# Optimization experiments

Hardware: AMD Instinct MI355X
Metric: run time of the kernel (lower is better)

Reference implementation:

```python
import jax, jax.numpy as jnp
import numpy as np

NEG = -9e15
SLOPE = 0.1  # LeakyReLU negative_slope in the torch module

B, N, NFEAT = 4, 2048, 256
NHID, NHEADS, NOUT = 64, 8, 128


def setup_inputs() -> dict:
    key = jax.random.key(0)
    ks = jax.random.split(key, 8)
    x = jax.random.normal(ks[0], (B, N, NFEAT), dtype=jnp.float32)
    adj = jax.random.randint(ks[1], (B, N, N), 0, 2, dtype=jnp.int32)
    s = 0.1
    Wh = jax.random.normal(ks[2], (NHEADS, NFEAT, NHID), dtype=jnp.float32) * s
    ah = jax.random.normal(ks[3], (NHEADS, 2 * NHID), dtype=jnp.float32) * s
    bh = jax.random.normal(ks[4], (NHEADS, NHID), dtype=jnp.float32) * s
    Wo = jax.random.normal(ks[5], (NHID * NHEADS, NOUT), dtype=jnp.float32) * s
    ao = jax.random.normal(ks[6], (2 * NOUT,), dtype=jnp.float32) * s
    bo = jax.random.normal(ks[7], (NOUT,), dtype=jnp.float32) * s
    return {"x": x, "adj": adj, "Wh": Wh, "ah": ah, "bh": bh,
            "Wo": Wo, "ao": ao, "bo": bo}


def _leaky(v):
    return jnp.where(v >= 0, v, SLOPE * v)


def _gat_layer(x, adj, W, a, b):
    # x: [B,N,Fin], W: [Fin,F], a: [2F], b: [F]
    h = jnp.einsum('bnf,fo->bno', x, W)          # [B,N,F]
    F = W.shape[1]
    a1, a2 = a[:F], a[F:]
    s1 = h @ a1                                   # [B,N] (query / row term)
    s2 = h @ a2                                   # [B,N] (key / col term)
    e = _leaky(s1[:, :, None] + s2[:, None, :])   # [B,N,N], avoids a_input blowup
    e = jnp.where(adj > 0, e, NEG)
    att = jax.nn.softmax(e, axis=2)               # [B,N,N]
    h_prime = jnp.einsum('bnm,bmf->bnf', att, h) + b
    return jax.nn.elu(h_prime)


def reference(x, adj, Wh, ah, bh, Wo, ao, bo):
    # per-head layers, vmapped over the head axis of the stacked params
    heads = jax.vmap(lambda W, a, b: _gat_layer(x, adj, W, a, b))(Wh, ah, bh)
    # [H,B,N,F] -> concat heads along feature dim: [B,N,H*F]
    hcat = jnp.transpose(heads, (1, 2, 0, 3)).reshape(x.shape[0], x.shape[1], -1)
    out = _gat_layer(hcat, adj, Wo, ao, bo)
    return jax.nn.relu(out)
```

## Files before the change

kernel.cpp:

```cpp
#include <hip/hip_runtime.h>

constexpr int B_ = 4;
constexpr int N_ = 2048;
constexpr int NFEAT_ = 256;
constexpr int NHEADS_ = 8;
constexpr float SLOPE_ = 0.1f;
constexpr float L2E = 1.4426950408889634f;

typedef __attribute__((ext_vector_type(8))) __fp16 f16x8;
typedef __attribute__((ext_vector_type(4))) __fp16 f16x4;
typedef __attribute__((ext_vector_type(2))) __fp16 f16x2;
typedef __attribute__((ext_vector_type(4))) float f32x4;

__device__ __forceinline__ f16x8 pack8(const float* v) {
  union { f16x2 h2[4]; f16x8 h8; } u;
  u.h2[0] = __builtin_amdgcn_cvt_pkrtz(v[0], v[1]);
  u.h2[1] = __builtin_amdgcn_cvt_pkrtz(v[2], v[3]);
  u.h2[2] = __builtin_amdgcn_cvt_pkrtz(v[4], v[5]);
  u.h2[3] = __builtin_amdgcn_cvt_pkrtz(v[6], v[7]);
  return u.h8;
}
__device__ __forceinline__ f16x4 pack4(float a, float b, float c, float d) {
  union { f16x2 h2[2]; f16x4 h4; } u;
  u.h2[0] = __builtin_amdgcn_cvt_pkrtz(a, b);
  u.h2[1] = __builtin_amdgcn_cvt_pkrtz(c, d);
  return u.h4;
}

__global__ __launch_bounds__(256) void k_prep(
    const int* __restrict__ adj, unsigned short* __restrict__ mask2,
    const float* __restrict__ Wh, __fp16* __restrict__ WhB,
    const float* __restrict__ Wo, __fp16* __restrict__ WoB)
{
  const int bid = blockIdx.x;
  const int l = threadIdx.x & 63;
  if (bid < 4096) {
    const size_t gw = ((size_t)bid * 256 + threadIdx.x) >> 6;
    const int jt = (int)(gw & 31);
    const int ig16 = (int)((gw >> 5) & 127);
    const int b = (int)(gw >> 12);
    const int q = l >> 4, c15 = l & 15;
    const int* base = adj + ((size_t)b * N_ + ig16 * 16) * N_ + jt * 64 + l;
    unsigned int msk = 0;
    #pragma unroll
    for (int r = 0; r < 16; ++r) {
      int a = base[(size_t)r * N_];
      unsigned long long bal = __ballot(a > 0);
      unsigned int v = (unsigned int)((bal >> (q * 8)) & 0xffull)
                     | ((unsigned int)((bal >> (q * 8 + 32)) & 0xffull) << 8);
      if (r == c15) msk = v;
    }
    mask2[gw * 64 + l] = (unsigned short)msk;
  } else if (bid < 4160) {
    int s = (int)(((bid - 4096) * 256 + threadIdx.x) >> 6);
    int h = s >> 5, ks = (s >> 2) & 7, ft = s & 3;
    const float* src = Wh + ((size_t)h * 256 + ks * 32 + (l >> 4) * 8) * 64 + ft * 16 + (l & 15);
    float v[8];
    #pragma unroll
    for (int j = 0; j < 8; ++j) v[j] = src[(size_t)j * 64];
    *(f16x8*)(WhB + (size_t)s * 512 + l * 8) = pack8(v);
  } else {
    int s = (int)(((bid - 4160) * 256 + threadIdx.x) >> 6);
    int ks = s >> 3, ft = s & 7;
    const float* src = Wo + ((size_t)ks * 32 + (l >> 4) * 8) * 128 + ft * 16 + (l & 15);
    float v[8];
    #pragma unroll
    for (int j = 0; j < 8; ++j) v[j] = src[(size_t)j * 128];
    *(f16x8*)(WoB + (size_t)s * 512 + l * 8) = pack8(v);
  }
}

__global__ __launch_bounds__(256, 4) void k_gemm1(
    const float* __restrict__ x, const __fp16* __restrict__ WhB,
    const float* __restrict__ ah,
    __fp16* __restrict__ hB1, float* __restrict__ s1h, float* __restrict__ s2h)
{
  constexpr int XP = 264;
  __shared__ __fp16 xs[16 * XP];
  __shared__ __fp16 hT[512 * 16];

  const int t = threadIdx.x;
  const int bid = blockIdx.x;
  const int b = bid >> 7;
  const int n0 = (bid & 127) * 16;

  {
    int r = t >> 4, k0 = (t & 15) * 16;
    const float* src = x + ((size_t)(b * N_) + n0 + r) * NFEAT_ + k0;
    float v0[8], v1[8];
    *(float4*)&v0[0] = *(const float4*)(src);
    *(float4*)&v0[4] = *(const float4*)(src + 4);
    *(float4*)&v1[0] = *(const float4*)(src + 8);
    *(float4*)&v1[4] = *(const float4*)(src + 12);
    *(f16x8*)&xs[r * XP + k0] = pack8(v0);
    *(f16x8*)&xs[r * XP + k0 + 8] = pack8(v1);
  }
  __syncthreads();

  const int w = t >> 6, l = t & 63;
  const int quad = l >> 4, c15 = l & 15;

  f32x4 acc[8];
  #pragma unroll
  for (int i = 0; i < 8; ++i) acc[i] = (f32x4){0.f, 0.f, 0.f, 0.f};

  for (int ks = 0; ks < 8; ++ks) {
    f16x8 af = *(const f16x8*)&xs[c15 * XP + ks * 32 + quad * 8];
    #pragma unroll
    for (int tt = 0; tt < 8; ++tt) {
      int hl = tt >> 2, ft = tt & 3;
      f16x8 bf = *(const f16x8*)(WhB +
          ((((size_t)(2 * w + hl) * 8 + ks) * 4 + ft) * 512) + l * 8);
      acc[tt] = __builtin_amdgcn_mfma_f32_16x16x32_f16(af, bf, acc[tt], 0, 0, 0);
    }
  }

  #pragma unroll
  for (int hl = 0; hl < 2; ++hl) {
    int head = 2 * w + hl;
    float a1v[4], a2v[4];
    #pragma unroll
    for (int ft = 0; ft < 4; ++ft) {
      a1v[ft] = ah[head * 128 + ft * 16 + c15] * L2E;
      a2v[ft] = ah[head * 128 + 64 + ft * 16 + c15] * L2E;
    }
    #pragma unroll
    for (int r = 0; r < 4; ++r) {
      float v1 = 0.f, v2 = 0.f;
      #pragma unroll
      for (int ft = 0; ft < 4; ++ft) {
        v1 = fmaf(acc[hl * 4 + ft][r], a1v[ft], v1);
        v2 = fmaf(acc[hl * 4 + ft][r], a2v[ft], v2);
      }
      #pragma unroll
      for (int off = 1; off < 16; off <<= 1) {
        v1 += __shfl_xor(v1, off, 64);
        v2 += __shfl_xor(v2, off, 64);
      }
      if (c15 == 0) {
        s1h[(size_t)(b * NHEADS_ + head) * N_ + n0 + quad * 4 + r] = v1;
        s2h[(size_t)(b * NHEADS_ + head) * N_ + n0 + quad * 4 + r] = v2;
      }
    }
  }

  #pragma unroll
  for (int tt = 0; tt < 8; ++tt) {
    int f = (2 * w + (tt >> 2)) * 64 + (tt & 3) * 16 + c15;
    *(f16x4*)&hT[f * 16 + quad * 4] =
        pack4(acc[tt][0], acc[tt][1], acc[tt][2], acc[tt][3]);
  }
  __syncthreads();

  const int base_oct = (n0 >> 3) & 3;
  #pragma unroll
  for (int q = 0; q < 4; ++q) {
    int s = t + q * 256;
    int c15v = s & 15, oct = (s >> 4) & 1, ft = (s >> 5) & 3, head = s >> 7;
    f16x8 v = *(const f16x8*)&hT[(head * 64 + ft * 16 + c15v) * 16 + oct * 8];
    int lane0 = (base_oct + oct) * 16 + c15v;
    *(f16x8*)(hB1 +
        ((((size_t)(b * NHEADS_ + head) * 64 + (n0 >> 5)) * 4 + ft) * 512) + lane0 * 8) = v;
  }
}

__global__ __launch_bounds__(256, 4) void k_gemm2(
    const __fp16* __restrict__ g1, const __fp16* __restrict__ WoB,
    const float* __restrict__ ao,
    __fp16* __restrict__ hB2, float* __restrict__ s1o, float* __restrict__ s2o)
{
  constexpr int GP = 520;
  __shared__ __fp16 gs[16 * GP];
  __shared__ __fp16 hT[128 * 16];
  __shared__ float sd1[4][16], sd2[4][16];

  const int t = threadIdx.x;
  const int bid = blockIdx.x;
  const int b = bid >> 7;
  const int n0 = (bid & 127) * 16;

  {
    int r = t >> 4, k0 = (t & 15) * 32;
    const __fp16* src = g1 + ((size_t)(b * N_) + n0 + r) * 512 + k0;
    #pragma unroll
    for (int i = 0; i < 4; ++i)
      *(f16x8*)&gs[r * GP + k0 + i * 8] = *(const f16x8*)(src + i * 8);
  }
  __syncthreads();

  const int w = t >> 6, l = t & 63;
  const int quad = l >> 4, c15 = l & 15;

  f32x4 acc[2];
  acc[0] = (f32x4){0.f, 0.f, 0.f, 0.f};
  acc[1] = (f32x4){0.f, 0.f, 0.f, 0.f};

  for (int ks = 0; ks < 16; ++ks) {
    f16x8 af = *(const f16x8*)&gs[c15 * GP + ks * 32 + quad * 8];
    #pragma unroll
    for (int tt = 0; tt < 2; ++tt) {
      int ft = 2 * w + tt;
      f16x8 bf = *(const f16x8*)(WoB + (((size_t)ks * 8 + ft) * 512) + l * 8);
      acc[tt] = __builtin_amdgcn_mfma_f32_16x16x32_f16(af, bf, acc[tt], 0, 0, 0);
    }
  }

  {
    float a1v[2], a2v[2];
    #pragma unroll
    for (int tt = 0; tt < 2; ++tt) {
      int f = (2 * w + tt) * 16 + c15;
      a1v[tt] = ao[f] * L2E;
      a2v[tt] = ao[128 + f] * L2E;
    }
    #pragma unroll
    for (int r = 0; r < 4; ++r) {
      float v1 = acc[0][r] * a1v[0] + acc[1][r] * a1v[1];
      float v2 = acc[0][r] * a2v[0] + acc[1][r] * a2v[1];
      #pragma unroll
      for (int off = 1; off < 16; off <<= 1) {
        v1 += __shfl_xor(v1, off, 64);
        v2 += __shfl_xor(v2, off, 64);
      }
      if (c15 == 0) { sd1[w][quad * 4 + r] = v1; sd2[w][quad * 4 + r] = v2; }
    }
  }

  #pragma unroll
  for (int tt = 0; tt < 2; ++tt) {
    int f = (2 * w + tt) * 16 + c15;
    *(f16x4*)&hT[f * 16 + quad * 4] =
        pack4(acc[tt][0], acc[tt][1], acc[tt][2], acc[tt][3]);
  }
  __syncthreads();

  if (t < 16)
    s1o[(size_t)b * N_ + n0 + t] = sd1[0][t] + sd1[1][t] + sd1[2][t] + sd1[3][t];
  else if (t < 32) {
    int rr = t - 16;
    s2o[(size_t)b * N_ + n0 + rr] = sd2[0][rr] + sd2[1][rr] + sd2[2][rr] + sd2[3][rr];
  }

  {
    int c15v = t & 15, oct = (t >> 4) & 1, ft = t >> 5;
    f16x8 v = *(const f16x8*)&hT[(ft * 16 + c15v) * 16 + oct * 8];
    int base_oct = (n0 >> 3) & 3;
    int lane0 = (base_oct + oct) * 16 + c15v;
    *(f16x8*)(hB2 +
        (((size_t)(b * 64 + (n0 >> 5)) * 8 + ft) * 512) + lane0 * 8) = v;
  }
}

__global__ __launch_bounds__(512, 4) void k_att1(
    const __fp16* __restrict__ hB, const float* __restrict__ s1,
    const float* __restrict__ s2, const unsigned short* __restrict__ mask2,
    const float* __restrict__ bias, __fp16* __restrict__ g1)
{
  constexpr int NRG = 4, NJQ = 2, JLEN = 1024, TJ = 64, NIT = JLEN / TJ;
  constexpr int TILE = TJ * 64;

  __shared__ __fp16 vbuf[NJQ][2][TILE];
  __shared__ float s2s[N_];
  __shared__ float red[8];

  const int tid = threadIdx.x;
  const int w = tid >> 6, l = tid & 63;
  const int quad = l >> 4, c15 = l & 15;
  const int rowg = w % NRG, jq = w / NRG;
  const int tc = rowg * 64 + l;

  int idx = blockIdx.x;
  const int ig = idx & 31; idx >>= 5;
  const int head = idx & 7;
  const int b = idx >> 3;
  const int i0w = ig * 64 + rowg * 16;

  const float* s1p = s1 + (size_t)(b * 8 + head) * N_;
  const float* s2p = s2 + (size_t)(b * 8 + head) * N_;
  const char* hBp = (const char*)(hB + (size_t)(b * 8 + head) * (N_ / 32) * 2048);
  const unsigned short* mp = mask2 + ((size_t)(b * 128 + (i0w >> 4)) * 32) * 64 + l;

  const int jbase = jq * JLEN;

  auto stage = [&](int j0, int slot) {
    const char* srcb = hBp + (size_t)(j0 >> 5) * 4096;
    #pragma unroll
    for (int c = 0; c < 2; ++c) {
      int off = (tc + c * 256) * 16;
      __builtin_amdgcn_global_load_lds(
          (const __attribute__((address_space(1))) unsigned int*)(srcb + off),
          (__attribute__((address_space(3))) unsigned int*)
              ((char*)&vbuf[jq][slot][0] + (off - l * 16)), 16, 0, 0);
    }
  };

  stage(jbase, 0);
  unsigned int mk = mp[(size_t)(jbase >> 6) * 64];

  float4 sv = *(const float4*)(s2p + tid * 4);
  *(float4*)&s2s[tid * 4] = sv;
  float lm = fmaxf(fmaxf(sv.x, sv.y), fmaxf(sv.z, sv.w));
  #pragma unroll
  for (int off = 1; off < 64; off <<= 1) lm = fmaxf(lm, __shfl_xor(lm, off, 64));
  if (l == 0) red[w] = lm;
  const float s1v = s1p[i0w + c15];
  __syncthreads();
  float s2m = red[0];
  #pragma unroll
  for (int q = 1; q < 8; ++q) s2m = fmaxf(s2m, red[q]);

  const float zm = s1v + s2m;
  const float m = fmaxf(zm, SLOPE_ * zm);
  const float p = s1v - m;
  const float cq = (SLOPE_ - 1.f) * m;

  f16x8 ones;
  #pragma unroll
  for (int i = 0; i < 8; ++i) ones[i] = (__fp16)1.0f;

  f32x4 acc[4], acc5;
  #pragma unroll
  for (int t = 0; t < 4; ++t) acc[t] = (f32x4){0.f, 0.f, 0.f, 0.f};
  acc5 = (f32x4){0.f, 0.f, 0.f, 0.f};

  for (int it = 0; it < NIT; ++it) {
    const int cur = it & 1;
    const int j0 = jbase + it * TJ;
    unsigned int nk = 0;
    if (it + 1 < NIT) {
      stage(j0 + TJ, cur ^ 1);
      nk = mp[(size_t)((j0 + TJ) >> 6) * 64];
    }

    #pragma unroll
    for (int h = 0; h < 2; ++h) {
      const int jk = j0 + h * 32;
      float s2r[8];
      *(float4*)&s2r[0] = *(const float4*)&s2s[jk + quad * 8];
      *(float4*)&s2r[4] = *(const float4*)&s2s[jk + quad * 8 + 4];
      const unsigned int mbyte = (mk >> (8 * h)) & 0xffu;
      float wgt[8];
      #pragma unroll
      for (int k = 0; k < 8; ++k) {
        float t0 = p + s2r[k];
        float t1 = fmaf(SLOPE_, t0, cq);
        float tm = fmaxf(t0, t1);
        float e = __builtin_amdgcn_exp2f(tm);
        int sel = (int)(mbyte << (31 - k)) >> 31;
        union { float f; int i; } u; u.f = e; u.i &= sel;
        wgt[k] = u.f;
      }
      f16x8 a = pack8(wgt);
      acc5 = __builtin_amdgcn_mfma_f32_16x16x32_f16(a, ones, acc5, 0, 0, 0);
      const __fp16* vb = &vbuf[jq][cur][h * 2048];
      #pragma unroll
      for (int t = 0; t < 4; ++t) {
        f16x8 bf = *(const f16x8*)(vb + t * 512 + l * 8);
        acc[t] = __builtin_amdgcn_mfma_f32_16x16x32_f16(a, bf, acc[t], 0, 0, 0);
      }
    }
    mk = nk;
    __syncthreads();
  }

  auto pacc = (float(*)[16][64])(&vbuf[0][0][0]);
  auto pls  = (float(*)[16])(&s2s[0]);
  if (jq == 1) {
    #pragma unroll
    for (int t = 0; t < 4; ++t)
      #pragma unroll
      for (int r = 0; r < 4; ++r)
        pacc[rowg][quad * 4 + r][t * 16 + c15] = acc[t][r];
    if (c15 == 0) {
      #pragma unroll
      for (int r = 0; r < 4; ++r) pls[rowg][quad * 4 + r] = acc5[r];
    }
  }
  __syncthreads();
  if (jq == 0) {
    float Lrow[4];
    #pragma unroll
    for (int r = 0; r < 4; ++r)
      Lrow[r] = acc5[r] + pls[rowg][quad * 4 + r];
    #pragma unroll
    for (int t = 0; t < 4; ++t)
      #pragma unroll
      for (int r = 0; r < 4; ++r)
        acc[t][r] += pacc[rowg][quad * 4 + r][t * 16 + c15];
    float lr[4];
    #pragma unroll
    for (int r = 0; r < 4; ++r) lr[r] = 1.f / Lrow[r];
    #pragma unroll
    for (int t = 0; t < 4; ++t) {
      const float bv = bias[head * 64 + t * 16 + c15];
      #pragma unroll
      for (int r = 0; r < 4; ++r) {
        const int i = i0w + quad * 4 + r;
        float v = acc[t][r] * lr[r] + bv;
        v = (v > 0.f) ? v : expm1f(v);
        g1[(size_t)(b * N_ + i) * 512 + head * 64 + t * 16 + c15] = (__fp16)v;
      }
    }
  }
}

__global__ __launch_bounds__(512, 4) void k_att2(
    const __fp16* __restrict__ hB, const float* __restrict__ s1,
    const float* __restrict__ s2, const unsigned short* __restrict__ mask2,
    const float* __restrict__ bias, float* __restrict__ out)
{
  constexpr int NRG = 2, NJQ = 4, JLEN = 512, TJ = 32, NIT = JLEN / TJ;
  constexpr int TILE = TJ * 64;

  __shared__ __fp16 vbuf[NJQ][2][TILE];
  __shared__ float s2s[N_];
  __shared__ float red[8];

  const int tid = threadIdx.x;
  const int w = tid >> 6, l = tid & 63;
  const int quad = l >> 4, c15 = l & 15;
  const int rowg = w % NRG, jq = w / NRG;
  const int tc = rowg * 64 + l;

  int idx = blockIdx.x;
  const int ig = idx & 63; idx >>= 6;
  const int fs = idx & 1;
  const int b = idx >> 1;
  const int i0w = ig * 32 + rowg * 16;

  const float* s1p = s1 + (size_t)b * N_;
  const float* s2p = s2 + (size_t)b * N_;
  const char* hBp = (const char*)(hB + (size_t)b * 64 * 4096 + fs * 2048);
  const unsigned short* mp = mask2 + ((size_t)(b * 128 + (i0w >> 4)) * 32) * 64 + l;

  const int jbase = jq * JLEN;

  auto stage = [&](int j0, int slot) {
    const char* srcb = hBp + (size_t)(j0 >> 5) * 8192;
    #pragma unroll
    for (int c = 0; c < 2; ++c) {
      int off = (tc + c * 128) * 16;
      __builtin_amdgcn_global_load_lds(
          (const __attribute__((address_space(1))) unsigned int*)(srcb + off),
          (__attribute__((address_space(3))) unsigned int*)
              ((char*)&vbuf[jq][slot][0] + (off - l * 16)), 16, 0, 0);
    }
  };

  stage(jbase, 0);
  unsigned int mk = mp[(size_t)(jbase >> 6) * 64];

  float4 sv = *(const float4*)(s2p + tid * 4);
  *(float4*)&s2s[tid * 4] = sv;
  float lm = fmaxf(fmaxf(sv.x, sv.y), fmaxf(sv.z, sv.w));
  #pragma unroll
  for (int off = 1; off < 64; off <<= 1) lm = fmaxf(lm, __shfl_xor(lm, off, 64));
  if (l == 0) red[w] = lm;
  const float s1v = s1p[i0w + c15];
  __syncthreads();
  float s2m = red[0];
  #pragma unroll
  for (int q = 1; q < 8; ++q) s2m = fmaxf(s2m, red[q]);

  const float zm = s1v + s2m;
  const float m = fmaxf(zm, SLOPE_ * zm);
  const float p = s1v - m;
  const float cq = (SLOPE_ - 1.f) * m;

  f16x8 ones;
  #pragma unroll
  for (int i = 0; i < 8; ++i) ones[i] = (__fp16)1.0f;

  f32x4 acc[4], acc5;
  #pragma unroll
  for (int t = 0; t < 4; ++t) acc[t] = (f32x4){0.f, 0.f, 0.f, 0.f};
  acc5 = (f32x4){0.f, 0.f, 0.f, 0.f};

  for (int it = 0; it < NIT; ++it) {
    const int cur = it & 1;
    const int j0 = jbase + it * TJ;
    unsigned int nk = 0;
    if (it + 1 < NIT) {
      stage(j0 + TJ, cur ^ 1);
      nk = mp[(size_t)((j0 + TJ) >> 6) * 64];
    }

    float s2r[8];
    *(float4*)&s2r[0] = *(const float4*)&s2s[j0 + quad * 8];
    *(float4*)&s2r[4] = *(const float4*)&s2s[j0 + quad * 8 + 4];
    const unsigned int mbyte = (mk >> (8 * ((j0 >> 5) & 1))) & 0xffu;
    float wgt[8];
    #pragma unroll
    for (int k = 0; k < 8; ++k) {
      float t0 = p + s2r[k];
      float t1 = fmaf(SLOPE_, t0, cq);
      float tm = fmaxf(t0, t1);
      float e = __builtin_amdgcn_exp2f(tm);
      int sel = (int)(mbyte << (31 - k)) >> 31;
      union { float f; int i; } u; u.f = e; u.i &= sel;
      wgt[k] = u.f;
    }
    f16x8 a = pack8(wgt);
    acc5 = __builtin_amdgcn_mfma_f32_16x16x32_f16(a, ones, acc5, 0, 0, 0);
    const __fp16* vb = &vbuf[jq][cur][0];
    #pragma unroll
    for (int t = 0; t < 4; ++t) {
      f16x8 bf = *(const f16x8*)(vb + t * 512 + l * 8);
      acc[t] = __builtin_amdgcn_mfma_f32_16x16x32_f16(a, bf, acc[t], 0, 0, 0);
    }
    mk = nk;
    __syncthreads();
  }

  auto pacc = (float(*)[NRG][16][64])(&vbuf[0][0][0]);
  auto pls  = (float(*)[NRG][16])(&s2s[0]);
  if (jq > 0) {
    #pragma unroll
    for (int t = 0; t < 4; ++t)
      #pragma unroll
      for (int r = 0; r < 4; ++r)
        pacc[jq - 1][rowg][quad * 4 + r][t * 16 + c15] = acc[t][r];
    if (c15 == 0) {
      #pragma unroll
      for (int r = 0; r < 4; ++r) pls[jq - 1][rowg][quad * 4 + r] = acc5[r];
    }
  }
  __syncthreads();
  if (jq == 0) {
    float Lrow[4];
    #pragma unroll
    for (int r = 0; r < 4; ++r) Lrow[r] = acc5[r];
    #pragma unroll
    for (int q = 0; q < NJQ - 1; ++q) {
      #pragma unroll
      for (int t = 0; t < 4; ++t)
        #pragma unroll
        for (int r = 0; r < 4; ++r)
          acc[t][r] += pacc[q][rowg][quad * 4 + r][t * 16 + c15];
      #pragma unroll
      for (int r = 0; r < 4; ++r) Lrow[r] += pls[q][rowg][quad * 4 + r];
    }
    float lr[4];
    #pragma unroll
    for (int r = 0; r < 4; ++r) lr[r] = 1.f / Lrow[r];
    #pragma unroll
    for (int t = 0; t < 4; ++t) {
      const float bv = bias[fs * 64 + t * 16 + c15];
      #pragma unroll
      for (int r = 0; r < 4; ++r) {
        const int i = i0w + quad * 4 + r;
        float v = acc[t][r] * lr[r] + bv;
        out[(size_t)(b * N_ + i) * 128 + fs * 64 + t * 16 + c15] = fmaxf(v, 0.f);
      }
    }
  }
}

extern "C" void kernel_launch(void* const* d_in, const int* in_sizes, int n_in,
                              void* d_out, int out_size, void* d_ws, size_t ws_size,
                              hipStream_t stream) {
  const float* x   = (const float*)d_in[0];
  const int*   adj = (const int*)d_in[1];
  const float* Wh  = (const float*)d_in[2];
  const float* ah  = (const float*)d_in[3];
  const float* bh  = (const float*)d_in[4];
  const float* Wo  = (const float*)d_in[5];
  const float* ao  = (const float*)d_in[6];
  const float* bo  = (const float*)d_in[7];
  float* out = (float*)d_out;

  float* ws   = (float*)d_ws;
  float* s1h  = ws;
  float* s2h  = s1h  + (size_t)B_ * NHEADS_ * N_;
  float* s1o  = s2h  + (size_t)B_ * NHEADS_ * N_;
  float* s2o  = s1o  + (size_t)B_ * N_;
  __fp16* g1  = (__fp16*)(s2o + (size_t)B_ * N_);
  __fp16* hB1 = g1  + (size_t)B_ * N_ * 512;
  __fp16* hB2 = hB1 + (size_t)B_ * NHEADS_ * N_ * 64;
  __fp16* WhB = hB2 + (size_t)B_ * N_ * 128;
  __fp16* WoB = WhB + (size_t)8 * 256 * 64;
  unsigned short* mask2 = (unsigned short*)(WoB + (size_t)512 * 128);

  k_prep<<<4192, 256, 0, stream>>>(adj, mask2, Wh, WhB, Wo, WoB);
  k_gemm1<<<B_ * (N_ / 16), 256, 0, stream>>>(x, WhB, ah, hB1, s1h, s2h);
  k_att1<<<B_ * NHEADS_ * (N_ / 64), 512, 0, stream>>>(
      hB1, s1h, s2h, mask2, bh, g1);
  k_gemm2<<<B_ * (N_ / 16), 256, 0, stream>>>(g1, WoB, ao, hB2, s1o, s2o);
  k_att2<<<B_ * 2 * (N_ / 32), 512, 0, stream>>>(
      hB2, s1o, s2o, mask2, bo, out);
}
```

Measured before the change: 198.1 us.

## Load value tiles directly from global into registers, dropping LDS double buffering

Both attention kernels stop staging the pre-swizzled h tiles into shared memory through async global-to-LDS copies with double buffering and per-iteration barriers. Each wave now loads its MFMA B-operand fragments straight from global memory (relying on L2/L1 reuse across waves and blocks), and the loop no longer needs __syncthreads. The partial-result reduction buffers become dedicated shared arrays instead of aliasing the old staging buffer. This removes barrier stalls and LDS traffic, but every wave now issues redundant global loads and latency hiding depends on the compiler and occupancy.

```diff
diff --git a/kernel.cpp b/kernel.cpp
--- a/kernel.cpp
+++ b/kernel.cpp
@@ -256,18 +256,17 @@
     const float* __restrict__ s2, const unsigned short* __restrict__ mask2,
     const float* __restrict__ bias, __fp16* __restrict__ g1)
 {
-  constexpr int NRG = 4, NJQ = 2, JLEN = 1024, TJ = 64, NIT = JLEN / TJ;
-  constexpr int TILE = TJ * 64;
-
-  __shared__ __fp16 vbuf[NJQ][2][TILE];
+  constexpr int NRG = 4, NJQ = 2, JLEN = 1024;
+
   __shared__ float s2s[N_];
   __shared__ float red[8];
+  __shared__ float pacc[NRG][16][64];
+  __shared__ float pls[NRG][16];
 
   const int tid = threadIdx.x;
   const int w = tid >> 6, l = tid & 63;
   const int quad = l >> 4, c15 = l & 15;
   const int rowg = w % NRG, jq = w / NRG;
-  const int tc = rowg * 64 + l;
 
   int idx = blockIdx.x;
   const int ig = idx & 31; idx >>= 5;
@@ -277,25 +276,10 @@
 
   const float* s1p = s1 + (size_t)(b * 8 + head) * N_;
   const float* s2p = s2 + (size_t)(b * 8 + head) * N_;
-  const char* hBp = (const char*)(hB + (size_t)(b * 8 + head) * (N_ / 32) * 2048);
+  const __fp16* hBp = hB + (size_t)(b * 8 + head) * (N_ / 32) * 2048 + l * 8;
   const unsigned short* mp = mask2 + ((size_t)(b * 128 + (i0w >> 4)) * 32) * 64 + l;
 
   const int jbase = jq * JLEN;
-
-  auto stage = [&](int j0, int slot) {
-    const char* srcb = hBp + (size_t)(j0 >> 5) * 4096;
-    #pragma unroll
-    for (int c = 0; c < 2; ++c) {
-      int off = (tc + c * 256) * 16;
-      __builtin_amdgcn_global_load_lds(
-          (const __attribute__((address_space(1))) unsigned int*)(srcb + off),
-          (__attribute__((address_space(3))) unsigned int*)
-              ((char*)&vbuf[jq][slot][0] + (off - l * 16)), 16, 0, 0);
-    }
-  };
-
-  stage(jbase, 0);
-  unsigned int mk = mp[(size_t)(jbase >> 6) * 64];
 
   float4 sv = *(const float4*)(s2p + tid * 4);
   *(float4*)&s2s[tid * 4] = sv;
@@ -323,18 +307,17 @@
   for (int t = 0; t < 4; ++t) acc[t] = (f32x4){0.f, 0.f, 0.f, 0.f};
   acc5 = (f32x4){0.f, 0.f, 0.f, 0.f};
 
-  for (int it = 0; it < NIT; ++it) {
-    const int cur = it & 1;
-    const int j0 = jbase + it * TJ;
-    unsigned int nk = 0;
-    if (it + 1 < NIT) {
-      stage(j0 + TJ, cur ^ 1);
-      nk = mp[(size_t)((j0 + TJ) >> 6) * 64];
-    }
-
+  for (int it = 0; it < JLEN / 64; ++it) {
+    const int j0 = jbase + it * 64;
+    const unsigned int mk = mp[(size_t)(j0 >> 6) * 64];
     #pragma unroll
     for (int h = 0; h < 2; ++h) {
       const int jk = j0 + h * 32;
+      const __fp16* vb = hBp + (size_t)(jk >> 5) * 2048;
+      f16x8 bf0 = *(const f16x8*)(vb);
+      f16x8 bf1 = *(const f16x8*)(vb + 512);
+      f16x8 bf2 = *(const f16x8*)(vb + 1024);
+      f16x8 bf3 = *(const f16x8*)(vb + 1536);
       float s2r[8];
       *(float4*)&s2r[0] = *(const float4*)&s2s[jk + quad * 8];
       *(float4*)&s2r[4] = *(const float4*)&s2s[jk + quad * 8 + 4];
@@ -352,19 +335,13 @@
       }
       f16x8 a = pack8(wgt);
       acc5 = __builtin_amdgcn_mfma_f32_16x16x32_f16(a, ones, acc5, 0, 0, 0);
-      const __fp16* vb = &vbuf[jq][cur][h * 2048];
-      #pragma unroll
-      for (int t = 0; t < 4; ++t) {
-        f16x8 bf = *(const f16x8*)(vb + t * 512 + l * 8);
-        acc[t] = __builtin_amdgcn_mfma_f32_16x16x32_f16(a, bf, acc[t], 0, 0, 0);
-      }
-    }
-    mk = nk;
-    __syncthreads();
-  }
-
-  auto pacc = (float(*)[16][64])(&vbuf[0][0][0]);
-  auto pls  = (float(*)[16])(&s2s[0]);
+      acc[0] = __builtin_amdgcn_mfma_f32_16x16x32_f16(a, bf0, acc[0], 0, 0, 0);
+      acc[1] = __builtin_amdgcn_mfma_f32_16x16x32_f16(a, bf1, acc[1], 0, 0, 0);
+      acc[2] = __builtin_amdgcn_mfma_f32_16x16x32_f16(a, bf2, acc[2], 0, 0, 0);
+      acc[3] = __builtin_amdgcn_mfma_f32_16x16x32_f16(a, bf3, acc[3], 0, 0, 0);
+    }
+  }
+
   if (jq == 1) {
     #pragma unroll
     for (int t = 0; t < 4; ++t)
@@ -409,18 +386,17 @@
     const float* __restrict__ s2, const unsigned short* __restrict__ mask2,
     const float* __restrict__ bias, float* __restrict__ out)
 {
-  constexpr int NRG = 2, NJQ = 4, JLEN = 512, TJ = 32, NIT = JLEN / TJ;
-  constexpr int TILE = TJ * 64;
-
-  __shared__ __fp16 vbuf[NJQ][2][TILE];
+  constexpr int NRG = 2, NJQ = 4, JLEN = 512;
+
   __shared__ float s2s[N_];
   __shared__ float red[8];
+  __shared__ float pacc[NJQ - 1][NRG][16][64];
+  __shared__ float pls[NJQ - 1][NRG][16];
 
   const int tid = threadIdx.x;
   const int w = tid >> 6, l = tid & 63;
   const int quad = l >> 4, c15 = l & 15;
   const int rowg = w % NRG, jq = w / NRG;
-  const int tc = rowg * 64 + l;
 
   int idx = blockIdx.x;
   const int ig = idx & 63; idx >>= 6;
@@ -430,25 +406,10 @@
 
   const float* s1p = s1 + (size_t)b * N_;
   const float* s2p = s2 + (size_t)b * N_;
-  const char* hBp = (const char*)(hB + (size_t)b * 64 * 4096 + fs * 2048);
+  const __fp16* hBp = hB + (size_t)b * 64 * 4096 + fs * 2048 + l * 8;
   const unsigned short* mp = mask2 + ((size_t)(b * 128 + (i0w >> 4)) * 32) * 64 + l;
 
   const int jbase = jq * JLEN;
-
-  auto stage = [&](int j0, int slot) {
-    const char* srcb = hBp + (size_t)(j0 >> 5) * 8192;
-    #pragma unroll
-    for (int c = 0; c < 2; ++c) {
-      int off = (tc + c * 128) * 16;
-      __builtin_amdgcn_global_load_lds(
-          (const __attribute__((address_space(1))) unsigned int*)(srcb + off),
-          (__attribute__((address_space(3))) unsigned int*)
-              ((char*)&vbuf[jq][slot][0] + (off - l * 16)), 16, 0, 0);
-    }
-  };
-
-  stage(jbase, 0);
-  unsigned int mk = mp[(size_t)(jbase >> 6) * 64];
 
   float4 sv = *(const float4*)(s2p + tid * 4);
   *(float4*)&s2s[tid * 4] = sv;
@@ -476,44 +437,41 @@
   for (int t = 0; t < 4; ++t) acc[t] = (f32x4){0.f, 0.f, 0.f, 0.f};
   acc5 = (f32x4){0.f, 0.f, 0.f, 0.f};
 
-  for (int it = 0; it < NIT; ++it) {
-    const int cur = it & 1;
-    const int j0 = jbase + it * TJ;
-    unsigned int nk = 0;
-    if (it + 1 < NIT) {
-      stage(j0 + TJ, cur ^ 1);
-      nk = mp[(size_t)((j0 + TJ) >> 6) * 64];
-    }
-
-    float s2r[8];
-    *(float4*)&s2r[0] = *(const float4*)&s2s[j0 + quad * 8];
-    *(float4*)&s2r[4] = *(const float4*)&s2s[j0 + quad * 8 + 4];
-    const unsigned int mbyte = (mk >> (8 * ((j0 >> 5) & 1))) & 0xffu;
-    float wgt[8];
-    #pragma unroll
-    for (int k = 0; k < 8; ++k) {
-      float t0 = p + s2r[k];
-      float t1 = fmaf(SLOPE_, t0, cq);
-      float tm = fmaxf(t0, t1);
-      float e = __builtin_amdgcn_exp2f(tm);
-      int sel = (int)(mbyte << (31 - k)) >> 31;
-      union { float f; int i; } u; u.f = e; u.i &= sel;
-      wgt[k] = u.f;
-    }
-    f16x8 a = pack8(wgt);
-    acc5 = __builtin_amdgcn_mfma_f32_16x16x32_f16(a, ones, acc5, 0, 0, 0);
-    const __fp16* vb = &vbuf[jq][cur][0];
-    #pragma unroll
-    for (int t = 0; t < 4; ++t) {
-      f16x8 bf = *(const f16x8*)(vb + t * 512 + l * 8);
-      acc[t] = __builtin_amdgcn_mfma_f32_16x16x32_f16(a, bf, acc[t], 0, 0, 0);
-    }
-    mk = nk;
-    __syncthreads();
-  }
-
-  auto pacc = (float(*)[NRG][16][64])(&vbuf[0][0][0]);
-  auto pls  = (float(*)[NRG][16])(&s2s[0]);
+  for (int it = 0; it < JLEN / 64; ++it) {
+    const int j0 = jbase + it * 64;
+    const unsigned int mk = mp[(size_t)(j0 >> 6) * 64];
+    #pragma unroll
+    for (int h = 0; h < 2; ++h) {
+      const int jk = j0 + h * 32;
+      const __fp16* vb = hBp + (size_t)(jk >> 5) * 4096;
+      f16x8 bf0 = *(const f16x8*)(vb);
+      f16x8 bf1 = *(const f16x8*)(vb + 512);
+      f16x8 bf2 = *(const f16x8*)(vb + 1024);
+      f16x8 bf3 = *(const f16x8*)(vb + 1536);
+      float s2r[8];
+      *(float4*)&s2r[0] = *(const float4*)&s2s[jk + quad * 8];
+      *(float4*)&s2r[4] = *(const float4*)&s2s[jk + quad * 8 + 4];
+      const unsigned int mbyte = (mk >> (8 * h)) & 0xffu;
+      float wgt[8];
+      #pragma unroll
+      for (int k = 0; k < 8; ++k) {
+        float t0 = p + s2r[k];
+        float t1 = fmaf(SLOPE_, t0, cq);
+        float tm = fmaxf(t0, t1);
+        float e = __builtin_amdgcn_exp2f(tm);
+        int sel = (int)(mbyte << (31 - k)) >> 31;
+        union { float f; int i; } u; u.f = e; u.i &= sel;
+        wgt[k] = u.f;
+      }
+      f16x8 a = pack8(wgt);
+      acc5 = __builtin_amdgcn_mfma_f32_16x16x32_f16(a, ones, acc5, 0, 0, 0);
+      acc[0] = __builtin_amdgcn_mfma_f32_16x16x32_f16(a, bf0, acc[0], 0, 0, 0);
+      acc[1] = __builtin_amdgcn_mfma_f32_16x16x32_f16(a, bf1, acc[1], 0, 0, 0);
+      acc[2] = __builtin_amdgcn_mfma_f32_16x16x32_f16(a, bf2, acc[2], 0, 0, 0);
+      acc[3] = __builtin_amdgcn_mfma_f32_16x16x32_f16(a, bf3, acc[3], 0, 0, 0);
+    }
+  }
+
   if (jq > 0) {
     #pragma unroll
     for (int t = 0; t < 4; ++t)
```

After: 209.9 us. +5.9%, slower.

## Compute attention weights in packed fp16 and stage V via registers

Applied to the files above, without the earlier changes.

Replaces the per-element fp32 LeakyReLU/exp2/mask chain with packed half-precision v_pk_fma/v_pk_max and v_exp_f16 through inline asm, using a small shared-memory LUT to expand mask bits into 16-bit lane masks. Also swaps the direct global-to-LDS async loads for register prefetch of the next V tile, written to LDS after the MFMAs. The goal is fewer VALU instructions per weight in the softmax-numerator path. In exchange it loses fp16 range and precision in the exponent argument and adds register pressure plus explicit LDS store traffic.

```diff
diff --git a/kernel.cpp b/kernel.cpp
--- a/kernel.cpp
+++ b/kernel.cpp
@@ -25,6 +25,23 @@
   u.h2[0] = __builtin_amdgcn_cvt_pkrtz(a, b);
   u.h2[1] = __builtin_amdgcn_cvt_pkrtz(c, d);
   return u.h4;
+}
+
+__device__ __forceinline__ unsigned int wpair(float za, float zb,
+                                              f16x2 sl2, f16x2 cq2,
+                                              unsigned int pm) {
+  f16x2 t0 = __builtin_amdgcn_cvt_pkrtz(za, zb);
+  f16x2 t1, tm;
+  asm("v_pk_fma_f16 %0, %1, %2, %3" : "=v"(t1) : "v"(sl2), "v"(t0), "v"(cq2));
+  asm("v_pk_max_f16 %0, %1, %2" : "=v"(tm) : "v"(t0), "v"(t1));
+  unsigned int utm;
+  __builtin_memcpy(&utm, &tm, 4);
+  unsigned int hi, elo, ehi, pk;
+  asm("v_lshrrev_b32 %0, 16, %1" : "=v"(hi) : "v"(utm));
+  asm("v_exp_f16 %0, %1" : "=v"(elo) : "v"(utm));
+  asm("v_exp_f16 %0, %1" : "=v"(ehi) : "v"(hi));
+  asm("v_pack_b32_f16 %0, %1, %2" : "=v"(pk) : "v"(elo), "v"(ehi));
+  return pk & pm;
 }
 
 __global__ __launch_bounds__(256) void k_prep(
@@ -262,6 +279,7 @@
   __shared__ __fp16 vbuf[NJQ][2][TILE];
   __shared__ float s2s[N_];
   __shared__ float red[8];
+  __shared__ uint2 mlut[16];
 
   const int tid = threadIdx.x;
   const int w = tid >> 6, l = tid & 63;
@@ -282,19 +300,18 @@
 
   const int jbase = jq * JLEN;
 
-  auto stage = [&](int j0, int slot) {
-    const char* srcb = hBp + (size_t)(j0 >> 5) * 4096;
-    #pragma unroll
-    for (int c = 0; c < 2; ++c) {
-      int off = (tc + c * 256) * 16;
-      __builtin_amdgcn_global_load_lds(
-          (const __attribute__((address_space(1))) unsigned int*)(srcb + off),
-          (__attribute__((address_space(3))) unsigned int*)
-              ((char*)&vbuf[jq][slot][0] + (off - l * 16)), 16, 0, 0);
-    }
-  };
-
-  stage(jbase, 0);
+  if (tid < 16) {
+    unsigned int v = tid;
+    mlut[tid] = (uint2){ ((v & 1u) ? 0xffffu : 0u) | ((v & 2u) ? 0xffff0000u : 0u),
+                         ((v & 4u) ? 0xffffu : 0u) | ((v & 8u) ? 0xffff0000u : 0u) };
+  }
+
+  float4 pf0, pf1;
+  {
+    const char* srcb = hBp + (size_t)(jbase >> 5) * 4096;
+    pf0 = *(const float4*)(srcb + tc * 16);
+    pf1 = *(const float4*)(srcb + (tc + 256) * 16);
+  }
   unsigned int mk = mp[(size_t)(jbase >> 6) * 64];
 
   float4 sv = *(const float4*)(s2p + tid * 4);
@@ -304,6 +321,8 @@
   for (int off = 1; off < 64; off <<= 1) lm = fmaxf(lm, __shfl_xor(lm, off, 64));
   if (l == 0) red[w] = lm;
   const float s1v = s1p[i0w + c15];
+  *(float4*)((char*)&vbuf[jq][0][0] + tc * 16) = pf0;
+  *(float4*)((char*)&vbuf[jq][0][0] + (tc + 256) * 16) = pf1;
   __syncthreads();
   float s2m = red[0];
   #pragma unroll
@@ -313,6 +332,8 @@
   const float m = fmaxf(zm, SLOPE_ * zm);
   const float p = s1v - m;
   const float cq = (SLOPE_ - 1.f) * m;
+  const f16x2 cq2 = __builtin_amdgcn_cvt_pkrtz(cq, cq);
+  const f16x2 sl2 = (f16x2){(__fp16)SLOPE_, (__fp16)SLOPE_};
 
   f16x8 ones;
   #pragma unroll
@@ -328,7 +349,9 @@
     const int j0 = jbase + it * TJ;
     unsigned int nk = 0;
     if (it + 1 < NIT) {
-      stage(j0 + TJ, cur ^ 1);
+      const char* srcb = hBp + (size_t)((j0 + TJ) >> 5) * 4096;
+      pf0 = *(const float4*)(srcb + tc * 16);
+      pf1 = *(const float4*)(srcb + (tc + 256) * 16);
       nk = mp[(size_t)((j0 + TJ) >> 6) * 64];
     }
 
@@ -339,18 +362,14 @@
       *(float4*)&s2r[0] = *(const float4*)&s2s[jk + quad * 8];
       *(float4*)&s2r[4] = *(const float4*)&s2s[jk + quad * 8 + 4];
       const unsigned int mbyte = (mk >> (8 * h)) & 0xffu;
-      float wgt[8];
-      #pragma unroll
-      for (int k = 0; k < 8; ++k) {
-        float t0 = p + s2r[k];
-        float t1 = fmaf(SLOPE_, t0, cq);
-        float tm = fmaxf(t0, t1);
-        float e = __builtin_amdgcn_exp2f(tm);
-        int sel = (int)(mbyte << (31 - k)) >> 31;
-        union { float f; int i; } u; u.f = e; u.i &= sel;
-        wgt[k] = u.f;
-      }
-      f16x8 a = pack8(wgt);
+      const uint2 mA = mlut[mbyte & 15u];
+      const uint2 mB = mlut[mbyte >> 4];
+      union { unsigned int u[4]; f16x8 v8; } af;
+      af.u[0] = wpair(p + s2r[0], p + s2r[1], sl2, cq2, mA.x);
+      af.u[1] = wpair(p + s2r[2], p + s2r[3], sl2, cq2, mA.y);
+      af.u[2] = wpair(p + s2r[4], p + s2r[5], sl2, cq2, mB.x);
+      af.u[3] = wpair(p + s2r[6], p + s2r[7], sl2, cq2, mB.y);
+      const f16x8 a = af.v8;
       acc5 = __builtin_amdgcn_mfma_f32_16x16x32_f16(a, ones, acc5, 0, 0, 0);
       const __fp16* vb = &vbuf[jq][cur][h * 2048];
       #pragma unroll
@@ -358,6 +377,12 @@
         f16x8 bf = *(const f16x8*)(vb + t * 512 + l * 8);
         acc[t] = __builtin_amdgcn_mfma_f32_16x16x32_f16(a, bf, acc[t], 0, 0, 0);
       }
+    }
+
+    if (it + 1 < NIT) {
+      char* dst = (char*)&vbuf[jq][cur ^ 1][0];
+      *(float4*)(dst + tc * 16) = pf0;
+      *(float4*)(dst + (tc + 256) * 16) = pf1;
     }
     mk = nk;
     __syncthreads();
@@ -415,6 +440,7 @@
   __shared__ __fp16 vbuf[NJQ][2][TILE];
   __shared__ float s2s[N_];
   __shared__ float red[8];
+  __shared__ uint2 mlut[16];
 
   const int tid = threadIdx.x;
   const int w = tid >> 6, l = tid & 63;
@@ -435,19 +461,18 @@
 
   const int jbase = jq * JLEN;
 
-  auto stage = [&](int j0, int slot) {
-    const char* srcb = hBp + (size_t)(j0 >> 5) * 8192;
-    #pragma unroll
-    for (int c = 0; c < 2; ++c) {
-      int off = (tc + c * 128) * 16;
-      __builtin_amdgcn_global_load_lds(
-          (const __attribute__((address_space(1))) unsigned int*)(srcb + off),
-          (__attribute__((address_space(3))) unsigned int*)
-              ((char*)&vbuf[jq][slot][0] + (off - l * 16)), 16, 0, 0);
-    }
-  };
-
-  stage(jbase, 0);
+  if (tid < 16) {
+    unsigned int v = tid;
+    mlut[tid] = (uint2){ ((v & 1u) ? 0xffffu : 0u) | ((v & 2u) ? 0xffff0000u : 0u),
+                         ((v & 4u) ? 0xffffu : 0u) | ((v & 8u) ? 0xffff0000u : 0u) };
+  }
+
+  float4 pf0, pf1;
+  {
+    const char* srcb = hBp + (size_t)(jbase >> 5) * 8192;
+    pf0 = *(const float4*)(srcb + tc * 16);
+    pf1 = *(const float4*)(srcb + (tc + 128) * 16);
+  }
   unsigned int mk = mp[(size_t)(jbase >> 6) * 64];
 
   float4 sv = *(const float4*)(s2p + tid * 4);
@@ -457,6 +482,8 @@
   for (int off = 1; off < 64; off <<= 1) lm = fmaxf(lm, __shfl_xor(lm, off, 64));
   if (l == 0) red[w] = lm;
   const float s1v = s1p[i0w + c15];
+  *(float4*)((char*)&vbuf[jq][0][0] + tc * 16) = pf0;
+  *(float4*)((char*)&vbuf[jq][0][0] + (tc + 128) * 16) = pf1;
   __syncthreads();
   float s2m = red[0];
   #pragma unroll
@@ -466,6 +493,8 @@
   const float m = fmaxf(zm, SLOPE_ * zm);
   const float p = s1v - m;
   const float cq = (SLOPE_ - 1.f) * m;
+  const f16x2 cq2 = __builtin_amdgcn_cvt_pkrtz(cq, cq);
+  const f16x2 sl2 = (f16x2){(__fp16)SLOPE_, (__fp16)SLOPE_};
 
   f16x8 ones;
   #pragma unroll
@@ -481,7 +510,9 @@
     const int j0 = jbase + it * TJ;
     unsigned int nk = 0;
     if (it + 1 < NIT) {
-      stage(j0 + TJ, cur ^ 1);
+      const char* srcb = hBp + (size_t)((j0 + TJ) >> 5) * 8192;
+      pf0 = *(const float4*)(srcb + tc * 16);
+      pf1 = *(const float4*)(srcb + (tc + 128) * 16);
       nk = mp[(size_t)((j0 + TJ) >> 6) * 64];
     }
 
@@ -489,24 +520,26 @@
     *(float4*)&s2r[0] = *(const float4*)&s2s[j0 + quad * 8];
     *(float4*)&s2r[4] = *(const float4*)&s2s[j0 + quad * 8 + 4];
     const unsigned int mbyte = (mk >> (8 * ((j0 >> 5) & 1))) & 0xffu;
-    float wgt[8];
-    #pragma unroll
-    for (int k = 0; k < 8; ++k) {
-      float t0 = p + s2r[k];
-      float t1 = fmaf(SLOPE_, t0, cq);
-      float tm = fmaxf(t0, t1);
-      float e = __builtin_amdgcn_exp2f(tm);
-      int sel = (int)(mbyte << (31 - k)) >> 31;
-      union { float f; int i; } u; u.f = e; u.i &= sel;
-      wgt[k] = u.f;
-    }
-    f16x8 a = pack8(wgt);
+    const uint2 mA = mlut[mbyte & 15u];
+    const uint2 mB = mlut[mbyte >> 4];
+    union { unsigned int u[4]; f16x8 v8; } af;
+    af.u[0] = wpair(p + s2r[0], p + s2r[1], sl2, cq2, mA.x);
+    af.u[1] = wpair(p + s2r[2], p + s2r[3], sl2, cq2, mA.y);
+    af.u[2] = wpair(p + s2r[4], p + s2r[5], sl2, cq2, mB.x);
+    af.u[3] = wpair(p + s2r[6], p + s2r[7], sl2, cq2, mB.y);
+    const f16x8 a = af.v8;
     acc5 = __builtin_amdgcn_mfma_f32_16x16x32_f16(a, ones, acc5, 0, 0, 0);
     const __fp16* vb = &vbuf[jq][cur][0];
     #pragma unroll
     for (int t = 0; t < 4; ++t) {
       f16x8 bf = *(const f16x8*)(vb + t * 512 + l * 8);
       acc[t] = __builtin_amdgcn_mfma_f32_16x16x32_f16(a, bf, acc[t], 0, 0, 0);
+    }
+
+    if (it + 1 < NIT) {
+      char* dst = (char*)&vbuf[jq][cur ^ 1][0];
+      *(float4*)(dst + tc * 16) = pf0;
+      *(float4*)(dst + (tc + 128) * 16) = pf1;
     }
     mk = nk;
     __syncthreads();
```

New measurement: 188.7 us. 4.8% less time.
